# Kernel optimization log

Measured on AMD Instinct MI355X. Metric: run time of the kernel, lower is better.

Reference implementation:

```python
import jax, jax.numpy as jnp
import numpy as np

D_MODEL = 1024
NUM_HEADS = 16
D_K = D_MODEL // NUM_HEADS
B, S = 2, 2048


def setup_inputs() -> dict:
    key = jax.random.key(0)
    ks = jax.random.split(key, 12)
    s = 1.0 / np.sqrt(D_MODEL)
    return {
        "query": jax.random.normal(ks[0], (B, S, D_MODEL), jnp.float32),
        "key": jax.random.normal(ks[1], (B, S, D_MODEL), jnp.float32),
        "value": jax.random.normal(ks[2], (B, S, D_MODEL), jnp.float32),
        "mask": jnp.ones((B, S), jnp.int32),
        "Wq": jax.random.uniform(ks[3], (D_MODEL, D_MODEL), jnp.float32, -s, s),
        "bq": jax.random.uniform(ks[4], (D_MODEL,), jnp.float32, -s, s),
        "Wk": jax.random.uniform(ks[5], (D_MODEL, D_MODEL), jnp.float32, -s, s),
        "bk": jax.random.uniform(ks[6], (D_MODEL,), jnp.float32, -s, s),
        "Wv": jax.random.uniform(ks[7], (D_MODEL, D_MODEL), jnp.float32, -s, s),
        "bv": jax.random.uniform(ks[8], (D_MODEL,), jnp.float32, -s, s),
        "Wo": jax.random.uniform(ks[9], (D_MODEL, D_MODEL), jnp.float32, -s, s),
        "bo": jax.random.uniform(ks[10], (D_MODEL,), jnp.float32, -s, s),
    }


def reference(query, key, value, mask, Wq, bq, Wk, bk, Wv, bv, Wo, bo):
    b, s, _ = query.shape
    scale = jnp.sqrt(jnp.asarray(D_K, jnp.float32)).astype(query.dtype)
    # QKV projections: x @ W.T + b (torch nn.Linear convention)
    Q = (query @ Wq.T + bq).reshape(b, s, NUM_HEADS, D_K).transpose(0, 2, 1, 3)
    K = (key @ Wk.T + bk).reshape(b, -1, NUM_HEADS, D_K).transpose(0, 2, 1, 3)
    V = (value @ Wv.T + bv).reshape(b, -1, NUM_HEADS, D_K).transpose(0, 2, 1, 3)
    # scores in fp32, then cast back to input dtype (matches source)
    scores = jnp.einsum('bhqd,bhkd->bhqk', Q.astype(jnp.float32), K.astype(jnp.float32)) / scale
    scores = scores.astype(Q.dtype)
    # 2D mask [B,S] -> [B,1,1,S], broadcast over heads/queries
    fill = jnp.finfo(scores.dtype).min
    scores = jnp.where(mask[:, None, None, :] == 0, fill, scores)
    attn = jax.nn.softmax(scores, axis=-1)  # dropout p=0 -> identity
    context = jnp.einsum('bhqk,bhkd->bhqd', attn, V)
    context = context.transpose(0, 2, 1, 3).reshape(b, s, D_MODEL)
    return context @ Wo.T + bo
```

## Files before the change

kernel.cpp:

```cpp
#include <hip/hip_runtime.h>


typedef __bf16 bf16_8 __attribute__((ext_vector_type(8)));
typedef __bf16 bf16_4 __attribute__((ext_vector_type(4)));
typedef float  f32x4  __attribute__((ext_vector_type(4)));

#define MFMA16(a, b, c) __builtin_amdgcn_mfma_f32_16x16x32_bf16((a), (b), (c), 0, 0, 0)

#if __has_builtin(__builtin_amdgcn_mfma_f32_16x16x16_bf16)
#define MFMA_PV(a, b, c) __builtin_amdgcn_mfma_f32_16x16x16_bf16((a), (b), (c), 0, 0, 0)
#elif __has_builtin(__builtin_amdgcn_mfma_f32_16x16x16bf16_1k)
typedef short s16x4 __attribute__((ext_vector_type(4)));
#define MFMA_PV(a, b, c)                                                  \
  __builtin_amdgcn_mfma_f32_16x16x16bf16_1k(                              \
      __builtin_bit_cast(s16x4, (a)), __builtin_bit_cast(s16x4, (b)), (c), 0, 0, 0)
#else
static __device__ __forceinline__ f32x4 mfma_pv_asm(bf16_4 a, bf16_4 b, f32x4 c) {
  asm volatile("v_mfma_f32_16x16x16_bf16 %0, %1, %2, %0\n\ts_nop 3"
               : "+v"(c) : "v"(a), "v"(b));
  return c;
}
#define MFMA_PV(a, b, c) mfma_pv_asm((a), (b), (c))
#endif

__device__ __forceinline__ void async_ld16(const void* g, void* l) {
  __builtin_amdgcn_global_load_lds(
      (__attribute__((address_space(1))) void*)g,
      (__attribute__((address_space(3))) void*)l, 16, 0, 0);
}

__device__ __forceinline__ void gemm_core_128(
    const __bf16* __restrict__ A, const __bf16* __restrict__ BT, int K,
    int tm, int tn, __bf16* At, __bf16* Bt, f32x4 acc[4][4]) {
  const int tid  = threadIdx.x;
  const int lane = tid & 63;
  const int w    = tid >> 6;
  const int quad = lane >> 4;
  const int c16  = lane & 15;
  const int wm = w >> 1, wn = w & 1;

  const int ch0  = w * 2;
  const int row0 = ch0 * 16 + (lane >> 2);
  const int col0 = (lane & 3) * 8;
  const __bf16* Ag = A  + (size_t)(tm + row0) * K + col0;
  const __bf16* Bg = BT + (size_t)(tn + row0) * K + col0;
  __bf16* Al = At + ch0 * 512;
  __bf16* Bl = Bt + ch0 * 512;
  const size_t rowK16 = (size_t)16 * K;

  for (int kt = 0; kt < K; kt += 32) {
    async_ld16(Ag + kt,          Al);
    async_ld16(Ag + rowK16 + kt, Al + 512);
    async_ld16(Bg + kt,          Bl);
    async_ld16(Bg + rowK16 + kt, Bl + 512);
    __syncthreads();

    bf16_8 af[4], bfr[4];
#pragma unroll
    for (int mi = 0; mi < 4; ++mi)
      af[mi] = *(const bf16_8*)(At + (wm * 64 + mi * 16 + c16) * 32 + quad * 8);
#pragma unroll
    for (int ni = 0; ni < 4; ++ni)
      bfr[ni] = *(const bf16_8*)(Bt + (wn * 64 + ni * 16 + c16) * 32 + quad * 8);
#pragma unroll
    for (int mi = 0; mi < 4; ++mi)
#pragma unroll
      for (int ni = 0; ni < 4; ++ni)
        acc[mi][ni] = MFMA16(af[mi], bfr[ni], acc[mi][ni]);
    __syncthreads();
  }
}

__global__ __launch_bounds__(256)
void qkv_fused(const __bf16* __restrict__ xq, const __bf16* __restrict__ xk,
               const __bf16* __restrict__ xv,
               const __bf16* __restrict__ wq, const __bf16* __restrict__ wk,
               const __bf16* __restrict__ wv,
               const float* __restrict__ bq, const float* __restrict__ bk,
               const float* __restrict__ bv,
               __bf16* __restrict__ Qo, __bf16* __restrict__ Ko,
               __bf16* __restrict__ Vo) {
  __shared__ __bf16 At[128 * 32];
  __shared__ __bf16 Bt[128 * 32];
  const int z  = blockIdx.z;
  const int bx = blockIdx.x;
  const __bf16 *A, *BT;
  const float* bias;
  int tm, tn;
  if (z == 2) {
    A = wv; BT = xv; bias = bv;
    tm = (bx >> 5) * 128; tn = (bx & 31) * 128;
  } else if (z == 1) {
    A = xk; BT = wk; bias = bk;
    tm = (bx >> 3) * 128; tn = (bx & 7) * 128;
  } else {
    A = xq; BT = wq; bias = bq;
    tm = (bx >> 3) * 128; tn = (bx & 7) * 128;
  }

  f32x4 acc[4][4];
  const f32x4 zero4 = {0.f, 0.f, 0.f, 0.f};
#pragma unroll
  for (int i = 0; i < 4; ++i)
#pragma unroll
    for (int j = 0; j < 4; ++j) acc[i][j] = zero4;

  gemm_core_128(A, BT, 1024, tm, tn, At, Bt, acc);

  const int lane = threadIdx.x & 63;
  const int w    = threadIdx.x >> 6;
  const int quad = lane >> 4, c16 = lane & 15;
  const int wm = w >> 1, wn = w & 1;

  if (z == 2) {
#pragma unroll
    for (int mi = 0; mi < 4; ++mi) {
#pragma unroll
      for (int ni = 0; ni < 4; ++ni) {
        const int n  = tn + wn * 64 + ni * 16 + c16;
        const int bb = n >> 11, s = n & 2047;
#pragma unroll
        for (int r = 0; r < 4; ++r) {
          const int m  = tm + wm * 64 + mi * 16 + quad * 4 + r;
          const int hh = m >> 6, d = m & 63;
          Vo[(((size_t)(bb * 16 + hh) * 64 + d) << 11) + s] =
              (__bf16)(acc[mi][ni][r] + bias[m]);
        }
      }
    }
  } else {
    __bf16* Out = (z == 1) ? Ko : Qo;
    const float scale = (z == 0) ? 0.125f : 1.0f;
#pragma unroll
    for (int mi = 0; mi < 4; ++mi) {
#pragma unroll
      for (int ni = 0; ni < 4; ++ni) {
        const int n  = tn + wn * 64 + ni * 16 + c16;
        const int hh = n >> 6, d = n & 63;
        const float bn = bias[n];
#pragma unroll
        for (int r = 0; r < 4; ++r) {
          const int m  = tm + wm * 64 + mi * 16 + quad * 4 + r;
          const int bb = m >> 11, s = m & 2047;
          Out[(((size_t)(bb * 16 + hh) * 2048 + s) << 6) + d] =
              (__bf16)((acc[mi][ni][r] + bn) * scale);
        }
      }
    }
  }
}

__global__ __launch_bounds__(256)
void out_proj(const __bf16* __restrict__ ctx, const __bf16* __restrict__ wo,
              const float* __restrict__ bo, float* __restrict__ out) {
  __shared__ __bf16 At[64 * 32];
  __shared__ __bf16 Bt[128 * 32];
  const int bx = blockIdx.x;
  const int tm = (bx >> 3) * 64, tn = (bx & 7) * 128;

  const int tid  = threadIdx.x;
  const int lane = tid & 63, w = tid >> 6;
  const int quad = lane >> 4, c16 = lane & 15;
  const int wm = w >> 1, wn = w & 1;

  const int row0 = lane >> 2, col0 = (lane & 3) * 8;
  const __bf16* Ag = ctx + (size_t)(tm + w * 16 + row0) * 1024 + col0;
  const __bf16* Bg = wo  + (size_t)(tn + w * 32 + row0) * 1024 + col0;
  __bf16* Al = At + w * 512;
  __bf16* Bl = Bt + w * 1024;

  f32x4 acc[2][4];
  const f32x4 zero4 = {0.f, 0.f, 0.f, 0.f};
#pragma unroll
  for (int i = 0; i < 2; ++i)
#pragma unroll
    for (int j = 0; j < 4; ++j) acc[i][j] = zero4;

  for (int kt = 0; kt < 1024; kt += 32) {
    async_ld16(Ag + kt, Al);
    async_ld16(Bg + kt, Bl);
    async_ld16(Bg + 16 * 1024 + kt, Bl + 512);
    __syncthreads();

    bf16_8 af[2], bfr[4];
#pragma unroll
    for (int mi = 0; mi < 2; ++mi)
      af[mi] = *(const bf16_8*)(At + (wm * 32 + mi * 16 + c16) * 32 + quad * 8);
#pragma unroll
    for (int ni = 0; ni < 4; ++ni)
      bfr[ni] = *(const bf16_8*)(Bt + (wn * 64 + ni * 16 + c16) * 32 + quad * 8);
#pragma unroll
    for (int mi = 0; mi < 2; ++mi)
#pragma unroll
      for (int ni = 0; ni < 4; ++ni)
        acc[mi][ni] = MFMA16(af[mi], bfr[ni], acc[mi][ni]);
    __syncthreads();
  }

#pragma unroll
  for (int mi = 0; mi < 2; ++mi) {
#pragma unroll
    for (int ni = 0; ni < 4; ++ni) {
      const int n = tn + wn * 64 + ni * 16 + c16;
      const float bn = bo[n];
#pragma unroll
      for (int r = 0; r < 4; ++r) {
        const int m = tm + wm * 32 + mi * 16 + quad * 4 + r;
        out[(size_t)m * 1024 + n] = acc[mi][ni][r] + bn;
      }
    }
  }
}

__global__ __launch_bounds__(128, 2)
void flash_attn(const __bf16* __restrict__ Qg, const __bf16* __restrict__ Kg,
                const __bf16* __restrict__ VTg, const int* __restrict__ maskg,
                __bf16* __restrict__ ctx) {
  __shared__ float Ored[64 * 68];
  __shared__ float lred[64];

  const int t    = threadIdx.x;
  const int lane = t & 63, w = t >> 6;
  const int quad = lane >> 4, c16 = lane & 15;
  const int qt = blockIdx.x, h = blockIdx.y, b = blockIdx.z;
  const size_t bh = (size_t)(b * 16 + h);
  const int qbase = qt * 64;

  bf16_8 aq[4][2];
#pragma unroll
  for (int qi = 0; qi < 4; ++qi) {
    const __bf16* qptr = Qg + (bh * 2048 + qbase + qi * 16 + c16) * 64;
    aq[qi][0] = *(const bf16_8*)(qptr + quad * 8);
    aq[qi][1] = *(const bf16_8*)(qptr + 32 + quad * 8);
  }

  f32x4 o[4][4];
  const f32x4 zero4 = {0.f, 0.f, 0.f, 0.f};
#pragma unroll
  for (int dt = 0; dt < 4; ++dt)
#pragma unroll
    for (int qi = 0; qi < 4; ++qi) o[dt][qi] = zero4;
  float lsum[4] = {0.f, 0.f, 0.f, 0.f};

  const __bf16* Kgp = Kg + bh * 2048 * 64;
  const __bf16* Vgp = VTg + bh * 64 * 2048;
  const int*    mgp = maskg + b * 2048;
  const float LOG2E  = 1.44269504088896f;
  const float SHIFT2 = -17.3123404907f;

  const int k0 = w * 1024;
  for (int kt = k0; kt < k0 + 1024; kt += 64) {
#pragma unroll
    for (int kb = 0; kb < 4; ++kb) {
      const int key0 = kt + kb * 16;
      const bf16_8 kf0 = *(const bf16_8*)&Kgp[(size_t)(key0 + c16) * 64 + quad * 8];
      const bf16_8 kf1 = *(const bf16_8*)&Kgp[(size_t)(key0 + c16) * 64 + 32 + quad * 8];
      const int4 mi4 = *(const int4*)&mgp[key0 + quad * 4];
      const float ma0 = mi4.x ? SHIFT2 : -1e30f;
      const float ma1 = mi4.y ? SHIFT2 : -1e30f;
      const float ma2 = mi4.z ? SHIFT2 : -1e30f;
      const float ma3 = mi4.w ? SHIFT2 : -1e30f;

      bf16_4 pf[4];
#pragma unroll
      for (int qi = 0; qi < 4; ++qi) {
        f32x4 sf = MFMA16(kf1, aq[qi][1], MFMA16(kf0, aq[qi][0], zero4));
        const float p0 = __builtin_amdgcn_exp2f(fmaf(sf[0], LOG2E, ma0));
        const float p1 = __builtin_amdgcn_exp2f(fmaf(sf[1], LOG2E, ma1));
        const float p2 = __builtin_amdgcn_exp2f(fmaf(sf[2], LOG2E, ma2));
        const float p3 = __builtin_amdgcn_exp2f(fmaf(sf[3], LOG2E, ma3));
        lsum[qi] += (p0 + p1) + (p2 + p3);
        bf16_4 pp = {(__bf16)p0, (__bf16)p1, (__bf16)p2, (__bf16)p3};
        pf[qi] = pp;
      }

#pragma unroll
      for (int dt = 0; dt < 4; ++dt) {
        const bf16_4 vf =
            *(const bf16_4*)&Vgp[(size_t)(dt * 16 + c16) * 2048 + key0 + quad * 4];
        o[dt][0] = MFMA_PV(vf, pf[0], o[dt][0]);
        o[dt][1] = MFMA_PV(vf, pf[1], o[dt][1]);
        o[dt][2] = MFMA_PV(vf, pf[2], o[dt][2]);
        o[dt][3] = MFMA_PV(vf, pf[3], o[dt][3]);
      }
    }
  }

#pragma unroll
  for (int qi = 0; qi < 4; ++qi) {
    float s_ = lsum[qi];
    s_ += __shfl_xor(s_, 16);
    s_ += __shfl_xor(s_, 32);
    lsum[qi] = s_;
  }

  if (w == 1) {
#pragma unroll
    for (int dt = 0; dt < 4; ++dt)
#pragma unroll
      for (int qi = 0; qi < 4; ++qi)
        *(f32x4*)&Ored[(qi * 16 + c16) * 68 + dt * 16 + quad * 4] = o[dt][qi];
    if (quad == 0) {
#pragma unroll
      for (int qi = 0; qi < 4; ++qi) lred[qi * 16 + c16] = lsum[qi];
    }
  }
  __syncthreads();
  if (w == 1) return;

  float rl[4];
#pragma unroll
  for (int qi = 0; qi < 4; ++qi)
    rl[qi] = 1.0f / (lsum[qi] + lred[qi * 16 + c16]);
#pragma unroll
  for (int dt = 0; dt < 4; ++dt)
#pragma unroll
    for (int qi = 0; qi < 4; ++qi)
      o[dt][qi] += *(const f32x4*)&Ored[(qi * 16 + c16) * 68 + dt * 16 + quad * 4];

  __bf16* Oe = (__bf16*)Ored;
#pragma unroll
  for (int dt = 0; dt < 4; ++dt) {
#pragma unroll
    for (int qi = 0; qi < 4; ++qi) {
      bf16_4 ob = {(__bf16)(o[dt][qi][0] * rl[qi]), (__bf16)(o[dt][qi][1] * rl[qi]),
                   (__bf16)(o[dt][qi][2] * rl[qi]), (__bf16)(o[dt][qi][3] * rl[qi])};
      *(bf16_4*)&Oe[(qi * 16 + c16) * 72 + dt * 16 + quad * 4] = ob;
    }
  }
  const int rr = lane >> 3, cc = lane & 7;
#pragma unroll
  for (int i = 0; i < 8; ++i) {
    const int q = i * 8 + rr;
    const bf16_8 val = *(const bf16_8*)&Oe[q * 72 + cc * 8];
    *(bf16_8*)&ctx[((size_t)b * 2048 + qbase + q) * 1024 + h * 64 + cc * 8] = val;
  }
}

__global__ __launch_bounds__(256)
void cvt_all(const float* __restrict__ q, const float* __restrict__ k,
             const float* __restrict__ v, const float* __restrict__ Wq,
             const float* __restrict__ Wk, const float* __restrict__ Wv,
             const float* __restrict__ Wo,
             __bf16* __restrict__ xq, __bf16* __restrict__ xk,
             __bf16* __restrict__ xv, __bf16* __restrict__ wqb,
             __bf16* __restrict__ wkb, __bf16* __restrict__ wvb,
             __bf16* __restrict__ wob) {
  const int y = blockIdx.y;
  const float* s;
  __bf16* d;
  int n8;
  switch (y) {
    case 0: s = q;  d = xq;  n8 = 524288; break;
    case 1: s = k;  d = xk;  n8 = 524288; break;
    case 2: s = v;  d = xv;  n8 = 524288; break;
    case 3: s = Wq; d = wqb; n8 = 131072; break;
    case 4: s = Wk; d = wkb; n8 = 131072; break;
    case 5: s = Wv; d = wvb; n8 = 131072; break;
    default: s = Wo; d = wob; n8 = 131072; break;
  }
  const int i = blockIdx.x * blockDim.x + threadIdx.x;
  if (i < n8) {
    const float4* sp = (const float4*)s;
    const float4 v0 = sp[i * 2], v1 = sp[i * 2 + 1];
    bf16_8 o;
    o[0] = (__bf16)v0.x; o[1] = (__bf16)v0.y;
    o[2] = (__bf16)v0.z; o[3] = (__bf16)v0.w;
    o[4] = (__bf16)v1.x; o[5] = (__bf16)v1.y;
    o[6] = (__bf16)v1.z; o[7] = (__bf16)v1.w;
    *(bf16_8*)(d + (size_t)i * 8) = o;
  }
}

extern "C" void kernel_launch(void* const* d_in, const int* in_sizes, int n_in,
                              void* d_out, int out_size, void* d_ws, size_t ws_size,
                              hipStream_t stream) {
  (void)in_sizes; (void)n_in; (void)out_size; (void)ws_size;
  const float* q    = (const float*)d_in[0];
  const float* k    = (const float*)d_in[1];
  const float* v    = (const float*)d_in[2];
  const int*   mask = (const int*)d_in[3];
  const float* Wq = (const float*)d_in[4];
  const float* bq = (const float*)d_in[5];
  const float* Wk = (const float*)d_in[6];
  const float* bk = (const float*)d_in[7];
  const float* Wv = (const float*)d_in[8];
  const float* bv = (const float*)d_in[9];
  const float* Wo = (const float*)d_in[10];
  const float* bo = (const float*)d_in[11];

  char* ws = (char*)d_ws;
  const size_t MB = 1ull << 20;
  __bf16* xq  = (__bf16*)(ws + 0 * MB);
  __bf16* xk  = (__bf16*)(ws + 8 * MB);
  __bf16* xv  = (__bf16*)(ws + 16 * MB);
  __bf16* wqb = (__bf16*)(ws + 24 * MB);
  __bf16* wkb = (__bf16*)(ws + 26 * MB);
  __bf16* wvb = (__bf16*)(ws + 28 * MB);
  __bf16* wob = (__bf16*)(ws + 30 * MB);
  __bf16* Qb  = (__bf16*)(ws + 32 * MB);
  __bf16* Kb  = (__bf16*)(ws + 40 * MB);
  __bf16* VTb = (__bf16*)(ws + 48 * MB);
  __bf16* ctx = (__bf16*)(ws + 56 * MB);

  cvt_all<<<dim3(2048, 7), 256, 0, stream>>>(q, k, v, Wq, Wk, Wv, Wo,
                                             xq, xk, xv, wqb, wkb, wvb, wob);

  qkv_fused<<<dim3(256, 1, 3), 256, 0, stream>>>(xq, xk, xv, wqb, wkb, wvb,
                                                 bq, bk, bv, Qb, Kb, VTb);

  flash_attn<<<dim3(32, 16, 2), 128, 0, stream>>>(Qb, Kb, VTb, mask, ctx);

  out_proj<<<dim3(512), 256, 0, stream>>>(ctx, wob, bo, (float*)d_out);
}
```

Baseline: 268.4 us.

## Split flash-attention key range across four waves with a tree reduction

The flash attention block grows from 2 to 4 waves, so each wave handles 512 keys instead of 1024. The partial outputs and row sums are combined with a two-step shared-memory tree reduction over two buffers. V fragment loads are also hoisted ahead of the QK/exp stage so their latency overlaps compute. The aim is more resident waves to hide global-load latency, at the cost of extra LDS traffic, an additional barrier and tighter register limits from the new launch bounds.

```diff
diff --git a/kernel.cpp b/kernel.cpp
--- a/kernel.cpp
+++ b/kernel.cpp
@@ -212,12 +212,13 @@
   }
 }
 
-__global__ __launch_bounds__(128, 2)
+__global__ __launch_bounds__(256, 4)
 void flash_attn(const __bf16* __restrict__ Qg, const __bf16* __restrict__ Kg,
                 const __bf16* __restrict__ VTg, const int* __restrict__ maskg,
                 __bf16* __restrict__ ctx) {
-  __shared__ float Ored[64 * 68];
-  __shared__ float lred[64];
+  __shared__ float bufA[64 * 68];
+  __shared__ float bufB[64 * 68];
+  __shared__ float lA[64], lB[64];
 
   const int t    = threadIdx.x;
   const int lane = t & 63, w = t >> 6;
@@ -248,14 +249,19 @@
   const float LOG2E  = 1.44269504088896f;
   const float SHIFT2 = -17.3123404907f;
 
-  const int k0 = w * 1024;
-  for (int kt = k0; kt < k0 + 1024; kt += 64) {
+  const int k0 = w * 512;
+  for (int kt = k0; kt < k0 + 512; kt += 64) {
 #pragma unroll
     for (int kb = 0; kb < 4; ++kb) {
       const int key0 = kt + kb * 16;
       const bf16_8 kf0 = *(const bf16_8*)&Kgp[(size_t)(key0 + c16) * 64 + quad * 8];
       const bf16_8 kf1 = *(const bf16_8*)&Kgp[(size_t)(key0 + c16) * 64 + 32 + quad * 8];
       const int4 mi4 = *(const int4*)&mgp[key0 + quad * 4];
+      bf16_4 vf[4];
+#pragma unroll
+      for (int dt = 0; dt < 4; ++dt)
+        vf[dt] = *(const bf16_4*)&Vgp[(size_t)(dt * 16 + c16) * 2048 + key0 + quad * 4];
+
       const float ma0 = mi4.x ? SHIFT2 : -1e30f;
       const float ma1 = mi4.y ? SHIFT2 : -1e30f;
       const float ma2 = mi4.z ? SHIFT2 : -1e30f;
@@ -276,12 +282,10 @@
 
 #pragma unroll
       for (int dt = 0; dt < 4; ++dt) {
-        const bf16_4 vf =
-            *(const bf16_4*)&Vgp[(size_t)(dt * 16 + c16) * 2048 + key0 + quad * 4];
-        o[dt][0] = MFMA_PV(vf, pf[0], o[dt][0]);
-        o[dt][1] = MFMA_PV(vf, pf[1], o[dt][1]);
-        o[dt][2] = MFMA_PV(vf, pf[2], o[dt][2]);
-        o[dt][3] = MFMA_PV(vf, pf[3], o[dt][3]);
+        o[dt][0] = MFMA_PV(vf[dt], pf[0], o[dt][0]);
+        o[dt][1] = MFMA_PV(vf[dt], pf[1], o[dt][1]);
+        o[dt][2] = MFMA_PV(vf[dt], pf[2], o[dt][2]);
+        o[dt][3] = MFMA_PV(vf[dt], pf[3], o[dt][3]);
       }
     }
   }
@@ -299,26 +303,68 @@
     for (int dt = 0; dt < 4; ++dt)
 #pragma unroll
       for (int qi = 0; qi < 4; ++qi)
-        *(f32x4*)&Ored[(qi * 16 + c16) * 68 + dt * 16 + quad * 4] = o[dt][qi];
+        *(f32x4*)&bufA[(qi * 16 + c16) * 68 + dt * 16 + quad * 4] = o[dt][qi];
     if (quad == 0) {
 #pragma unroll
-      for (int qi = 0; qi < 4; ++qi) lred[qi * 16 + c16] = lsum[qi];
+      for (int qi = 0; qi < 4; ++qi) lA[qi * 16 + c16] = lsum[qi];
+    }
+  }
+  if (w == 3) {
+#pragma unroll
+    for (int dt = 0; dt < 4; ++dt)
+#pragma unroll
+      for (int qi = 0; qi < 4; ++qi)
+        *(f32x4*)&bufB[(qi * 16 + c16) * 68 + dt * 16 + quad * 4] = o[dt][qi];
+    if (quad == 0) {
+#pragma unroll
+      for (int qi = 0; qi < 4; ++qi) lB[qi * 16 + c16] = lsum[qi];
     }
   }
   __syncthreads();
-  if (w == 1) return;
-
+  if (w == 0) {
+#pragma unroll
+    for (int dt = 0; dt < 4; ++dt)
+#pragma unroll
+      for (int qi = 0; qi < 4; ++qi)
+        o[dt][qi] += *(const f32x4*)&bufA[(qi * 16 + c16) * 68 + dt * 16 + quad * 4];
+#pragma unroll
+    for (int qi = 0; qi < 4; ++qi) lsum[qi] += lA[qi * 16 + c16];
+  }
+  if (w == 2) {
+#pragma unroll
+    for (int dt = 0; dt < 4; ++dt)
+#pragma unroll
+      for (int qi = 0; qi < 4; ++qi)
+        o[dt][qi] += *(const f32x4*)&bufB[(qi * 16 + c16) * 68 + dt * 16 + quad * 4];
+#pragma unroll
+    for (int qi = 0; qi < 4; ++qi) lsum[qi] += lB[qi * 16 + c16];
+  }
+  __syncthreads();
+  if (w == 2) {
+#pragma unroll
+    for (int dt = 0; dt < 4; ++dt)
+#pragma unroll
+      for (int qi = 0; qi < 4; ++qi)
+        *(f32x4*)&bufA[(qi * 16 + c16) * 68 + dt * 16 + quad * 4] = o[dt][qi];
+    if (quad == 0) {
+#pragma unroll
+      for (int qi = 0; qi < 4; ++qi) lA[qi * 16 + c16] = lsum[qi];
+    }
+  }
+  __syncthreads();
+  if (w != 0) return;
+
+#pragma unroll
+  for (int dt = 0; dt < 4; ++dt)
+#pragma unroll
+    for (int qi = 0; qi < 4; ++qi)
+      o[dt][qi] += *(const f32x4*)&bufA[(qi * 16 + c16) * 68 + dt * 16 + quad * 4];
   float rl[4];
 #pragma unroll
   for (int qi = 0; qi < 4; ++qi)
-    rl[qi] = 1.0f / (lsum[qi] + lred[qi * 16 + c16]);
-#pragma unroll
-  for (int dt = 0; dt < 4; ++dt)
-#pragma unroll
-    for (int qi = 0; qi < 4; ++qi)
-      o[dt][qi] += *(const f32x4*)&Ored[(qi * 16 + c16) * 68 + dt * 16 + quad * 4];
-
-  __bf16* Oe = (__bf16*)Ored;
+    rl[qi] = 1.0f / (lsum[qi] + lA[qi * 16 + c16]);
+
+  __bf16* Oe = (__bf16*)bufB;
 #pragma unroll
   for (int dt = 0; dt < 4; ++dt) {
 #pragma unroll
@@ -409,7 +455,7 @@
   qkv_fused<<<dim3(256, 1, 3), 256, 0, stream>>>(xq, xk, xv, wqb, wkb, wvb,
                                                  bq, bk, bv, Qb, Kb, VTb);
 
-  flash_attn<<<dim3(32, 16, 2), 128, 0, stream>>>(Qb, Kb, VTb, mask, ctx);
+  flash_attn<<<dim3(32, 16, 2), 256, 0, stream>>>(Qb, Kb, VTb, mask, ctx);
 
   out_proj<<<dim3(512), 256, 0, stream>>>(ctx, wob, bo, (float*)d_out);
 }
```

Result: slower. 629.6 us (+134.6%).
